# Optimization experiments

Hardware: AMD Instinct MI355X
Metric: run time of the kernel (lower is better)

The kernel has to match this reference:

```python
import jax, jax.numpy as jnp
import numpy as np

N_NODES = 100000
N_EDGES = 400000
HIDDEN = 128
HEADS = 8
HEAD_DIM = HIDDEN // HEADS


def _lin_params(key, d_in, d_out):
    kw, kb = jax.random.split(key)
    s = 1.0 / np.sqrt(d_in)
    W = jax.random.uniform(kw, (d_in, d_out), jnp.float32, -s, s)
    b = jax.random.uniform(kb, (d_out,), jnp.float32, -s, s)
    return W, b


def setup_inputs() -> dict:
    key = jax.random.key(0)
    ks = jax.random.split(key, 12)
    inp = {
        "x": jax.random.normal(ks[0], (N_NODES, HIDDEN), jnp.float32),
        "edge_attr": jax.random.normal(ks[1], (N_EDGES, HIDDEN), jnp.float32),
        "edge_index": jax.random.randint(ks[2], (2, N_EDGES), 0, N_NODES, dtype=jnp.int32),
        "batch": jnp.zeros((N_NODES,), jnp.int32),
    }
    names = ["Q", "K", "V", "Ew", "Eb", "Ev", "O", "Eo"]
    for i, nm in enumerate(names):
        W, b = _lin_params(ks[3 + i], HIDDEN, HIDDEN)
        inp[f"W_{nm}"] = W
        inp[f"b_{nm}"] = b
    WA, bA = _lin_params(ks[11], HIDDEN, HEADS)
    inp["W_A"] = WA
    inp["b_A"] = bA
    return inp


def signed_sqrt(x):
    return jnp.sign(x) * jnp.sqrt(jnp.abs(x) + 1e-8)


def reference(x, edge_attr, edge_index, batch,
              W_Q, b_Q, W_K, b_K, W_V, b_V,
              W_Ew, b_Ew, W_Eb, b_Eb, W_Ev, b_Ev,
              W_O, b_O, W_Eo, b_Eo, W_A, b_A):
    n = x.shape[0]
    e = edge_index.shape[1]
    h, hd = HEADS, HEAD_DIM
    src, tgt = edge_index[0], edge_index[1]

    Q = (x @ W_Q + b_Q).reshape(n, h, hd)
    K = (x @ W_K + b_K).reshape(n, h, hd)
    V = (x @ W_V + b_V).reshape(n, h, hd)

    # edge-gathered attention features [E, H, HD]
    attn_feat = Q[src] + K[tgt]
    E_w = (edge_attr @ W_Ew + b_Ew).reshape(e, h, hd)
    E_b = (edge_attr @ W_Eb + b_Eb).reshape(e, h, hd)
    attn_feat = signed_sqrt(attn_feat * E_w) + E_b
    attn_feat = jax.nn.relu(attn_feat)

    # per-head scores [E, H], segment softmax over target node
    scores = attn_feat.reshape(e, h * hd) @ W_A + b_A
    seg_max = jax.ops.segment_max(scores, tgt, num_segments=n)
    ex = jnp.exp(scores - seg_max[tgt])
    seg_sum = jax.ops.segment_sum(ex, tgt, num_segments=n)
    alpha = ex / (seg_sum[tgt] + 1e-16)  # [E, H]

    a = alpha[:, :, None]
    E_v = (edge_attr @ W_Ev + b_Ev).reshape(e, h, hd)
    messages = V[src] * a + E_v * a  # [E, H, HD]

    agg = jax.ops.segment_sum(messages, tgt, num_segments=n).reshape(n, h * hd)
    x_out = agg @ W_O + b_O
    edge_attr_out = attn_feat.reshape(e, h * hd) @ W_Eo + b_Eo
    return x_out, edge_attr_out
```

## Files before the change

### kernel.cpp

```cpp
#include <hip/hip_runtime.h>
#include <hip/hip_bf16.h>

typedef __hip_bfloat16 bf16;

#define N_NODES 100000
#define N_EDGES 400000
#define EO_MIN  100000

#define OUT_E_ELEM ((size_t)N_NODES*128)
#define SCORES_B   ((size_t)N_EDGES*8*4)
#define SEG_B      ((size_t)N_NODES*8*4)
#define AGG_BYTES  ((size_t)N_NODES*128*4)
#define WSW_OFF    (SCORES_B + 2*SEG_B)

#define WT_SZ   16384
#define OFF_WQ  (0*WT_SZ)
#define OFF_WK  (2*WT_SZ)
#define OFF_WEW (4*WT_SZ)
#define OFF_WEB (6*WT_SZ)
#define OFF_WEO (8*WT_SZ)
#define OFF_WV  (10*WT_SZ)
#define OFF_WEV (12*WT_SZ)
#define OFF_WA  (14*WT_SZ)
#define WSW_SHORTS (14*WT_SZ + 2*2048)
#define WSW_BYTES  ((size_t)WSW_SHORTS*2)

using short8 = __attribute__((ext_vector_type(8))) short;
using f32x4  = __attribute__((ext_vector_type(4))) float;

__device__ __forceinline__ float b2f(bf16 v){ return __bfloat162float(v); }
__device__ __forceinline__ bf16  f2b(float v){ return __float2bfloat16(v); }
__device__ __forceinline__ short bits(bf16 v){ short s; __builtin_memcpy(&s, &v, 2); return s; }
__device__ __forceinline__ void split(float v, short& h, short& l){
  bf16 hb = f2b(v);
  h = bits(hb);
  l = bits(f2b(v - b2f(hb)));
}
__device__ __forceinline__ float san(float v){
  return (v == v && fabsf(v) < 1e30f) ? v : 0.f;
}
__device__ __forceinline__ unsigned fmap(float f){
  unsigned u = __float_as_uint(f);
  return (u & 0x80000000u) ? ~u : (u | 0x80000000u);
}
__device__ __forceinline__ float funmap(unsigned u){
  unsigned b = (u & 0x80000000u) ? (u ^ 0x80000000u) : ~u;
  return __uint_as_float(b);
}

__global__ void prep_v18(const float* __restrict__ W_Q, const float* __restrict__ W_K,
                         const float* __restrict__ W_Ew, const float* __restrict__ W_Eb,
                         const float* __restrict__ W_Eo, const float* __restrict__ W_V,
                         const float* __restrict__ W_Ev, const float* __restrict__ W_A,
                         short* __restrict__ wsw)
{
  const int b = blockIdx.x;
  if (b < 896){
    const int mi = b >> 7, n = b & 127;
    const float* W = (mi==0)?W_Q:(mi==1)?W_K:(mi==2)?W_Ew:(mi==3)?W_Eb:(mi==4)?W_Eo:(mi==5)?W_V:W_Ev;
    short* dh = wsw + mi*2*WT_SZ;
    short* dl = dh + WT_SZ;
    for (int k = threadIdx.x; k < 128; k += 128){
      short h, l; split(W[(size_t)k*128 + n], h, l);
      dh[n*128 + k] = h; dl[n*128 + k] = l;
    }
  } else {
    const int n = b - 896;
    short* dh = wsw + OFF_WA;
    short* dl = dh + 2048;
    for (int k = threadIdx.x; k < 128; k += 128){
      float v = (n < 8) ? W_A[(size_t)k*8 + n] : 0.f;
      short h, l; split(v, h, l);
      dh[n*128 + k] = h; dl[n*128 + k] = l;
    }
  }
}

__device__ __forceinline__ void stage_row(const float* __restrict__ src,
                                          short* __restrict__ dh, short* __restrict__ dl){
  const float4 v0 = *reinterpret_cast<const float4*>(src);
  const float4 v1 = *reinterpret_cast<const float4*>(src + 4);
  const float vv[8] = {v0.x, v0.y, v0.z, v0.w, v1.x, v1.y, v1.z, v1.w};
  short8 h, l;
  #pragma unroll
  for (int q = 0; q < 8; ++q){ short hh, ll; split(vv[q], hh, ll); h[q] = hh; l[q] = ll; }
  *reinterpret_cast<short8*>(dh) = h;
  *reinterpret_cast<short8*>(dl) = l;
}

__global__ __launch_bounds__(256) void nodeproj_v18(
    const float* __restrict__ x, const short* __restrict__ wsw,
    const float* __restrict__ b_Q, const float* __restrict__ b_K,
    const float* __restrict__ b_V,
    float* __restrict__ Qn, float* __restrict__ Kn, float* __restrict__ Vn,
    int do_v)
{
  __shared__ __align__(16) short Xh[2][2048], Xl[2][2048];
  const int tid = threadIdx.x;
  const int n0  = blockIdx.x * 32;

  {
    const int r = tid & 15, c = tid >> 4;
    #pragma unroll
    for (int rg = 0; rg < 2; ++rg)
      stage_row(x + (size_t)(n0 + rg*16 + r)*128 + c*8,
                &Xh[rg][(c*16 + r)*8], &Xl[rg][(c*16 + r)*8]);
  }
  __syncthreads();

  const int wv = tid >> 6;
  const int mi = (tid & 63) & 15;
  const int kg = (tid & 63) >> 4;

  f32x4 aQ[2][2], aK[2][2], aV[2][2];
  #pragma unroll
  for (int rg = 0; rg < 2; ++rg)
    #pragma unroll
    for (int t = 0; t < 2; ++t){
      aQ[rg][t] = (f32x4){0,0,0,0}; aK[rg][t] = (f32x4){0,0,0,0}; aV[rg][t] = (f32x4){0,0,0,0};
    }

  #pragma unroll
  for (int ks = 0; ks < 4; ++ks){
// ... 17 lines not shown
      #pragma unroll
      for (int rg = 0; rg < 2; ++rg){
        aQ[rg][t] = __builtin_amdgcn_mfma_f32_16x16x32_bf16(xh[rg], qh, aQ[rg][t], 0,0,0);
        aK[rg][t] = __builtin_amdgcn_mfma_f32_16x16x32_bf16(xh[rg], kh, aK[rg][t], 0,0,0);
        aQ[rg][t] = __builtin_amdgcn_mfma_f32_16x16x32_bf16(xl[rg], qh, aQ[rg][t], 0,0,0);
        aK[rg][t] = __builtin_amdgcn_mfma_f32_16x16x32_bf16(xl[rg], kh, aK[rg][t], 0,0,0);
        aQ[rg][t] = __builtin_amdgcn_mfma_f32_16x16x32_bf16(xh[rg], ql, aQ[rg][t], 0,0,0);
        aK[rg][t] = __builtin_amdgcn_mfma_f32_16x16x32_bf16(xh[rg], kl, aK[rg][t], 0,0,0);
        if (do_v){
          aV[rg][t] = __builtin_amdgcn_mfma_f32_16x16x32_bf16(xh[rg], vh, aV[rg][t], 0,0,0);
          aV[rg][t] = __builtin_amdgcn_mfma_f32_16x16x32_bf16(xl[rg], vh, aV[rg][t], 0,0,0);
          aV[rg][t] = __builtin_amdgcn_mfma_f32_16x16x32_bf16(xh[rg], vl, aV[rg][t], 0,0,0);
        }
      }
    }
  }

  #pragma unroll
  for (int rg = 0; rg < 2; ++rg)
    #pragma unroll
    for (int t = 0; t < 2; ++t){
      const int n = (wv*2 + t)*16 + mi;
      const float bq = b_Q[n], bk = b_K[n], bv = b_V[n];
      #pragma unroll
      for (int q = 0; q < 4; ++q){
        const size_t row = n0 + rg*16 + kg*4 + q;
        Qn[row*128 + n] = aQ[rg][t][q] + bq;
        Kn[row*128 + n] = aK[rg][t][q] + bk;
        if (do_v) Vn[row*128 + n] = aV[rg][t][q] + bv;
      }
    }
}

__global__ __launch_bounds__(256) void front_qk_v18(
    const float* __restrict__ ea, const int* __restrict__ eidx,
    const float* __restrict__ Qn, const float* __restrict__ Kn,
    const float* __restrict__ b_Ew, const float* __restrict__ b_Eb,
    const float* __restrict__ b_A,  const float* __restrict__ b_Eo,
    const short* __restrict__ wsw,
    float* __restrict__ scores, unsigned* __restrict__ segmax,
    float* __restrict__ oute, int do_score)
{
  __shared__ __align__(16) char smem[16384];
  __shared__ int sIdx[32], tIdx[32];
  short* AFh = (short*)smem;
  short* AFl = (short*)(smem + 8192);
  float* qkf = (float*)smem;

  const int tid = threadIdx.x;
  const int e0  = blockIdx.x * 32;

  if (tid < 32){
    sIdx[tid] = eidx[e0 + tid];
    tIdx[tid] = eidx[N_EDGES + e0 + tid];
  }
  {
    const int r = tid & 15, c = tid >> 4;
    #pragma unroll
    for (int rg = 0; rg < 2; ++rg)
      stage_row(ea + (size_t)(e0 + rg*16 + r)*128 + c*8,
                &AFh[rg*2048 + (c*16 + r)*8], &AFl[rg*2048 + (c*16 + r)*8]);
  }
  __syncthreads();

  const int wv = tid >> 6;
  const int mi = (tid & 63) & 15;
  const int kg = (tid & 63) >> 4;

  f32x4 aw[2][2], ab[2][2];
  #pragma unroll
  for (int rg = 0; rg < 2; ++rg)
    #pragma unroll
    for (int t = 0; t < 2; ++t){ aw[rg][t] = (f32x4){0,0,0,0}; ab[rg][t] = (f32x4){0,0,0,0}; }

  #pragma unroll
  for (int ks = 0; ks < 4; ++ks){
    const int ao = ((ks*4 + kg)*16 + mi)*8;
    const int kb = ks*32 + kg*8;
    short8 eh[2], el_[2];
    #pragma unroll
    for (int rg = 0; rg < 2; ++rg){
      eh[rg]  = *reinterpret_cast<const short8*>(&AFh[rg*2048 + ao]);
      el_[rg] = *reinterpret_cast<const short8*>(&AFl[rg*2048 + ao]);
    }
    #pragma unroll
    for (int t = 0; t < 2; ++t){
      const int n = (wv*2 + t)*16 + mi;
      const short8 wh = *reinterpret_cast<const short8*>(&wsw[OFF_WEW + n*128 + kb]);
      const short8 wl = *reinterpret_cast<const short8*>(&wsw[OFF_WEW + WT_SZ + n*128 + kb]);
      const short8 bh = *reinterpret_cast<const short8*>(&wsw[OFF_WEB + n*128 + kb]);
      const short8 bl = *reinterpret_cast<const short8*>(&wsw[OFF_WEB + WT_SZ + n*128 + kb]);
      #pragma unroll
      for (int rg = 0; rg < 2; ++rg){
        aw[rg][t] = __builtin_amdgcn_mfma_f32_16x16x32_bf16(eh[rg], wh, aw[rg][t], 0,0,0);
        ab[rg][t] = __builtin_amdgcn_mfma_f32_16x16x32_bf16(eh[rg], bh, ab[rg][t], 0,0,0);
        aw[rg][t] = __builtin_amdgcn_mfma_f32_16x16x32_bf16(el_[rg], wh, aw[rg][t], 0,0,0);
        ab[rg][t] = __builtin_amdgcn_mfma_f32_16x16x32_bf16(el_[rg], bh, ab[rg][t], 0,0,0);
        aw[rg][t] = __builtin_amdgcn_mfma_f32_16x16x32_bf16(eh[rg], wl, aw[rg][t], 0,0,0);
        ab[rg][t] = __builtin_amdgcn_mfma_f32_16x16x32_bf16(eh[rg], bl, ab[rg][t], 0,0,0);
      }
    }
  }
  __syncthreads();

  {
    const int r = tid >> 3, cg = tid & 7;
    const float* qp = Qn + (size_t)sIdx[r]*128 + cg*16;
    const float* kp = Kn + (size_t)tIdx[r]*128 + cg*16;
    #pragma unroll
    for (int p = 0; p < 4; ++p){
      const float4 qv = *reinterpret_cast<const float4*>(qp + p*4);
      const float4 kv = *reinterpret_cast<const float4*>(kp + p*4);
      float4 s; s.x = qv.x+kv.x; s.y = qv.y+kv.y; s.z = qv.z+kv.z; s.w = qv.w+kv.w;
      *reinterpret_cast<float4*>(&qkf[r*128 + cg*16 + p*4]) = s;
    }
  }
  __syncthreads();

  short afh[2][2][4], afl[2][2][4];
  #pragma unroll
  for (int rg = 0; rg < 2; ++rg)
    #pragma unroll
    for (int t = 0; t < 2; ++t){
      const int n = (wv*2 + t)*16 + mi;
      const float bw = b_Ew[n], bb = b_Eb[n];
      #pragma unroll
      for (int q = 0; q < 4; ++q){
        const float qkv = qkf[(rg*16 + kg*4 + q)*128 + n];
        const float ew  = aw[rg][t][q] + bw;
        const float eb  = ab[rg][t][q] + bb;
        const float pre = qkv * ew;
        const float ssv = pre > 0.f ?  sqrtf( pre + 1e-8f)
                        : (pre < 0.f ? -sqrtf(-pre + 1e-8f) : 0.f);
        const float af = fmaxf(ssv + eb, 0.f);
        short hh, ll; split(af, hh, ll);
        afh[rg][t][q] = hh; afl[rg][t][q] = ll;
      }
    }
  __syncthreads();

  #pragma unroll
  for (int rg = 0; rg < 2; ++rg)
    #pragma unroll
    for (int t = 0; t < 2; ++t){
      const int c  = (wv*2 + t)*2 + (mi >> 3);
      const int k7 = mi & 7;
      #pragma unroll
// ... 27 lines not shown
        const int er = rg*16 + kg*4 + q;
        const float s = san(acc[q] + ba);
        scores[(size_t)(e0 + er)*8 + mi] = s;
        atomicMax(&segmax[(size_t)tIdx[er]*8 + mi], fmap(s));
      }
    }
  }

  #pragma unroll
  for (int rg = 0; rg < 2; ++rg)
    #pragma unroll
    for (int t2 = 0; t2 < 2; ++t2){
      const int n = (wv*2 + t2)*16 + mi;
      f32x4 acc = {0,0,0,0};
      #pragma unroll
      for (int ks = 0; ks < 4; ++ks){
        const int kb = ks*32 + kg*8;
        const int ao = ((ks*4 + kg)*16 + mi)*8;
        const short8 ah = *reinterpret_cast<const short8*>(&AFh[rg*2048 + ao]);
        const short8 al = *reinterpret_cast<const short8*>(&AFl[rg*2048 + ao]);
        const short8 bh = *reinterpret_cast<const short8*>(&wsw[OFF_WEO + n*128 + kb]);
        const short8 bl = *reinterpret_cast<const short8*>(&wsw[OFF_WEO + WT_SZ + n*128 + kb]);
        acc = __builtin_amdgcn_mfma_f32_16x16x32_bf16(ah, bh, acc, 0,0,0);
        acc = __builtin_amdgcn_mfma_f32_16x16x32_bf16(al, bh, acc, 0,0,0);
        acc = __builtin_amdgcn_mfma_f32_16x16x32_bf16(ah, bl, acc, 0,0,0);
      }
      const float be = b_Eo[n];
      #pragma unroll
      for (int q = 0; q < 4; ++q)
        oute[(size_t)(e0 + rg*16 + kg*4 + q)*128 + n] = san(acc[q] + be);
    }
}

__global__ __launch_bounds__(256) void seg_sum_v18(const float* __restrict__ scores,
    const int* __restrict__ eidx, const unsigned* __restrict__ segmax,
    float* __restrict__ segsum)
{
  int i = blockIdx.x*256 + threadIdx.x;
  if (i >= N_EDGES*8) return;
  int e = i >> 3, h = i & 7;
  int t = eidx[N_EDGES + e];
  float m = funmap(segmax[(size_t)t*8 + h]);
  atomicAdd(&segsum[(size_t)t*8 + h], expf(scores[i] - m));
}

__global__ __launch_bounds__(256) void messages_mfma_v18(
    const float* __restrict__ ea, const int* __restrict__ eidx,
    const float* __restrict__ Vn, const float* __restrict__ b_Ev,
    const short* __restrict__ wsw,
    const float* __restrict__ scores, const unsigned* __restrict__ segmax,
    float* __restrict__ den, float* __restrict__ agg)
{
  __shared__ __align__(16) short Eh[2][2048], El[2][2048];
  __shared__ int sIdx[32], tIdx[32];

  const int tid = threadIdx.x;
  const int e0  = blockIdx.x * 32;

  if (tid < 32){
    sIdx[tid] = eidx[e0 + tid];
    tIdx[tid] = eidx[N_EDGES + e0 + tid];
  }
  {
    const int r = tid & 15, c = tid >> 4;
    #pragma unroll
    for (int rg = 0; rg < 2; ++rg)
      stage_row(ea + (size_t)(e0 + rg*16 + r)*128 + c*8,
                &Eh[rg][(c*16 + r)*8], &El[rg][(c*16 + r)*8]);
  }
  __syncthreads();

  const int wv = tid >> 6;
  const int mi = (tid & 63) & 15;
  const int kg = (tid & 63) >> 4;

  f32x4 aev[2][2];
  #pragma unroll
  for (int rg = 0; rg < 2; ++rg)
    #pragma unroll
    for (int t = 0; t < 2; ++t) aev[rg][t] = (f32x4){0,0,0,0};

  #pragma unroll
  for (int ks = 0; ks < 4; ++ks){
    const int ao = ((ks*4 + kg)*16 + mi)*8;
    const int kb = ks*32 + kg*8;
    short8 eh[2], el_[2];
    #pragma unroll
    for (int rg = 0; rg < 2; ++rg){
      eh[rg]  = *reinterpret_cast<const short8*>(&Eh[rg][ao]);
      el_[rg] = *reinterpret_cast<const short8*>(&El[rg][ao]);
    }
    #pragma unroll
    for (int t = 0; t < 2; ++t){
      const int n = (wv*2 + t)*16 + mi;
      const short8 bh = *reinterpret_cast<const short8*>(&wsw[OFF_WEV + n*128 + kb]);
      const short8 bl = *reinterpret_cast<const short8*>(&wsw[OFF_WEV + WT_SZ + n*128 + kb]);
      #pragma unroll
      for (int rg = 0; rg < 2; ++rg){
        aev[rg][t] = __builtin_amdgcn_mfma_f32_16x16x32_bf16(eh[rg], bh, aev[rg][t], 0,0,0);
        aev[rg][t] = __builtin_amdgcn_mfma_f32_16x16x32_bf16(el_[rg], bh, aev[rg][t], 0,0,0);
        aev[rg][t] = __builtin_amdgcn_mfma_f32_16x16x32_bf16(eh[rg], bl, aev[rg][t], 0,0,0);
      }
    }
  }

  #pragma unroll
  for (int rg = 0; rg < 2; ++rg)
    #pragma unroll
    for (int t = 0; t < 2; ++t){
      const int n = (wv*2 + t)*16 + mi;
      const int h = n >> 4;
      const float be = b_Ev[n];
      #pragma unroll
      for (int q = 0; q < 4; ++q){
        const int row = rg*16 + kg*4 + q;
        const size_t e = (size_t)e0 + row;
        const int s = sIdx[row], tg = tIdx[row];
        const float m    = funmap(segmax[(size_t)tg*8 + h]);
        const float expw = expf(scores[e*8 + h] - m);
        const float msg  = san((Vn[(size_t)s*128 + n] + aev[rg][t][q] + be) * expw);
        atomicAdd(&agg[(size_t)tg*128 + n], msg);
        if (mi == 0) atomicAdd(&den[(size_t)tg*8 + h], expw);
      }
    }
}

__global__ __launch_bounds__(256) void messages_v14f(
    const float* __restrict__ x, const float* __restrict__ ea,
    const int* __restrict__ eidx,
    const float* __restrict__ W_V,  const float* __restrict__ b_V,
    const float* __restrict__ W_Ev, const float* __restrict__ b_Ev,
    const float* __restrict__ scores, const unsigned* __restrict__ segmax,
    const float* __restrict__ segsum, float* __restrict__ agg)
{
  __shared__ float eaT[128][16], xsT[128][16];
  __shared__ int sIdx[16], tIdx[16];

  const int tid = threadIdx.x;
  const int e0  = blockIdx.x * 16;

  if (tid < 16){
    sIdx[tid] = eidx[e0 + tid];
    tIdx[tid] = eidx[N_EDGES + e0 + tid];
  }
  __syncthreads();

  for (int idx = tid; idx < 16*128; idx += 256){
    int r = idx >> 7, k = idx & 127;
    eaT[k][r] = ea[(size_t)(e0 + r)*128 + k];
    xsT[k][r] = x[(size_t)sIdx[r]*128 + k];
  }
  __syncthreads();

  const int j  = tid & 127;
  const int h8 = (tid >> 7) * 8;
// ... 3 lines not shown
  for (int i=0;i<8;i++){ av[i]=0.f; ae[i]=0.f; }

  for (int k=0;k<128;k++){
    const float wv = W_V[(size_t)k*128 + j];
    const float we = W_Ev[(size_t)k*128 + j];
    const float4 s0 = *reinterpret_cast<const float4*>(&xsT[k][h8]);
    const float4 s1 = *reinterpret_cast<const float4*>(&xsT[k][h8+4]);
    const float4 e0v = *reinterpret_cast<const float4*>(&eaT[k][h8]);
    const float4 e1v = *reinterpret_cast<const float4*>(&eaT[k][h8+4]);
    const float sv[8] = {s0.x,s0.y,s0.z,s0.w,s1.x,s1.y,s1.z,s1.w};
    const float ev[8] = {e0v.x,e0v.y,e0v.z,e0v.w,e1v.x,e1v.y,e1v.z,e1v.w};
    #pragma unroll
    for (int i=0;i<8;i++){
      av[i] = fmaf(sv[i], wv, av[i]);
      ae[i] = fmaf(ev[i], we, ae[i]);
    }
  }

  const float bv = b_V[j], be = b_Ev[j];
  const int h = j >> 4;
  #pragma unroll
  for (int i=0;i<8;i++){
    const int el = h8 + i;
    const size_t e = (size_t)e0 + el;
    const int t = tIdx[el];
    const float m   = funmap(segmax[(size_t)t*8 + h]);
    const float d   = segsum[(size_t)t*8 + h] + 1e-16f;
    const float a   = expf(scores[e*8 + h] - m) / d;
    const float msg = san(((av[i] + bv) + (ae[i] + be)) * a);
    atomicAdd(&agg[(size_t)t*128 + j], msg);
  }
}

__global__ __launch_bounds__(256) void oproj_v18(const float* __restrict__ agg,
    const float* __restrict__ den,
    const float* __restrict__ W, const float* __restrict__ bias,
    float* __restrict__ outx)
{
  __shared__ float AT[128][32];
  const int tid  = threadIdx.x;
  const int base = blockIdx.x * 32;

  for (int idx = tid; idx < 32*128; idx += 256){
    int r = idx >> 7, k = idx & 127;
    float v = agg[(size_t)(base + r)*128 + k];
    if (den) v /= (den[(size_t)(base + r)*8 + (k >> 4)] + 1e-16f);
    AT[k][r] = v;
  }
  __syncthreads();

  const int j  = tid & 127;
  const int rb = (tid >> 7) * 16;
  float acc[16];
  #pragma unroll
  for (int i=0;i<16;i++) acc[i] = 0.f;

  for (int k=0;k<128;k++){
    const float w = W[(size_t)k*128 + j];
    const float4 a0 = *reinterpret_cast<const float4*>(&AT[k][rb]);
    const float4 a1 = *reinterpret_cast<const float4*>(&AT[k][rb+4]);
    const float4 a2 = *reinterpret_cast<const float4*>(&AT[k][rb+8]);
    const float4 a3 = *reinterpret_cast<const float4*>(&AT[k][rb+12]);
    const float avv[16] = {a0.x,a0.y,a0.z,a0.w,a1.x,a1.y,a1.z,a1.w,
                           a2.x,a2.y,a2.z,a2.w,a3.x,a3.y,a3.z,a3.w};
    #pragma unroll
    for (int i=0;i<16;i++) acc[i] = fmaf(avv[i], w, acc[i]);
  }

  const float bj = bias[j];
  #pragma unroll
  for (int i=0;i<16;i++)
    outx[(size_t)(base + rb + i)*128 + j] = san(acc[i] + bj);
}

template<bool PREPPED>
__global__ __launch_bounds__(256) void front_v14f(
    const float* __restrict__ x, const float* __restrict__ ea,
    const int* __restrict__ eidx,
    const float* __restrict__ W_Q, const float* __restrict__ b_Q,
    const float* __restrict__ W_K, const float* __restrict__ b_K,
// ... 172 lines not shown
        acc = __builtin_amdgcn_mfma_f32_16x16x32_bf16(ah, bh, acc, 0,0,0);
        acc = __builtin_amdgcn_mfma_f32_16x16x32_bf16(al, bh, acc, 0,0,0);
        acc = __builtin_amdgcn_mfma_f32_16x16x32_bf16(ah, bl, acc, 0,0,0);
      }
      const float be = b_Eo[n];
      #pragma unroll
      for (int q = 0; q < 4; ++q)
        oute[(size_t)(e0 + kg*4 + q)*128 + n] = san(acc[q] + be);
    }
  }
}

extern "C" void kernel_launch(void* const* d_in, const int* in_sizes, int n_in,
                              void* d_out, int out_size, void* d_ws, size_t ws_size,
                              hipStream_t stream)
{
  (void)in_sizes; (void)n_in; (void)out_size;
  const float* x    = (const float*)d_in[0];
  const float* ea   = (const float*)d_in[1];
  const int*   eidx = (const int*)d_in[2];
  const float* W_Q  = (const float*)d_in[4];  const float* b_Q  = (const float*)d_in[5];
  const float* W_K  = (const float*)d_in[6];  const float* b_K  = (const float*)d_in[7];
  const float* W_V  = (const float*)d_in[8];  const float* b_V  = (const float*)d_in[9];
  const float* W_Ew = (const float*)d_in[10]; const float* b_Ew = (const float*)d_in[11];
  const float* W_Eb = (const float*)d_in[12]; const float* b_Eb = (const float*)d_in[13];
  const float* W_Ev = (const float*)d_in[14]; const float* b_Ev = (const float*)d_in[15];
  const float* W_O  = (const float*)d_in[16]; const float* b_O  = (const float*)d_in[17];
  const float* W_Eo = (const float*)d_in[18]; const float* b_Eo = (const float*)d_in[19];
  const float* W_A  = (const float*)d_in[20]; const float* b_A  = (const float*)d_in[21];

  float* out_x = (float*)d_out;
  float* oute  = out_x + OUT_E_ELEM;

  float*    scores = (float*)d_out;
  unsigned* segmax = (unsigned*)((char*)d_out + SCORES_B);
  float*    segsum = (float*)((char*)d_out + SCORES_B + SEG_B);

  const size_t SZ_NODEF = (size_t)N_NODES*128*4;
  const size_t NEED_QK   = 2*SZ_NODEF + WSW_BYTES;
  const size_t NEED_FULL = 3*SZ_NODEF + WSW_BYTES;

  const int tier = (ws_size >= NEED_FULL) ? 2 : (ws_size >= NEED_QK) ? 1 : 0;

  dim3 blk(256);
  hipMemsetAsync((void*)segmax, 0, 2*SEG_B, stream);

  if (tier >= 1){
    char*  ws  = (char*)d_ws;
    float* Qn  = (float*)ws;
    float* Kn  = (float*)(ws + SZ_NODEF);
    float* Vn  = (tier == 2) ? (float*)(ws + 2*SZ_NODEF) : nullptr;
    short* wsw = (short*)(ws + ((tier == 2) ? 3 : 2)*SZ_NODEF);
    float* agg = Qn;
    float* den = Kn;

    prep_v18<<<dim3(912), dim3(128), 0, stream>>>(W_Q, W_K, W_Ew, W_Eb, W_Eo, W_V, W_Ev, W_A, wsw);

    nodeproj_v18<<<dim3(N_NODES/32), blk, 0, stream>>>(x, wsw, b_Q, b_K, b_V,
        Qn, Kn, Vn, tier == 2 ? 1 : 0);

    front_qk_v18<<<dim3(N_EDGES/32), blk, 0, stream>>>(ea, eidx, Qn, Kn,
        b_Ew, b_Eb, b_A, b_Eo, wsw, scores, segmax, oute, 1);

    hipMemsetAsync((void*)agg, 0, AGG_BYTES + SEG_B, stream);

    if (tier == 2){
      messages_mfma_v18<<<dim3(N_EDGES/32), blk, 0, stream>>>(ea, eidx, Vn, b_Ev,
          wsw, scores, segmax, den, agg);
      oproj_v18<<<dim3(N_NODES/32), blk, 0, stream>>>(agg, den, W_O, b_O, out_x);
    } else {
      seg_sum_v18<<<dim3((N_EDGES*8 + 255)/256), blk, 0, stream>>>(scores, eidx, segmax, segsum);
      messages_v14f<<<dim3(N_EDGES/16), blk, 0, stream>>>(x, ea, eidx,
          W_V, b_V, W_Ev, b_Ev, scores, segmax, segsum, agg);
      oproj_v18<<<dim3(N_NODES/32), blk, 0, stream>>>(agg, nullptr, W_O, b_O, out_x);
    }

  } else {
    short* wsw = (short*)((char*)d_out + WSW_OFF);
    float* agg = oute;

    hipMemsetAsync((void*)agg, 0, AGG_BYTES, stream);

    prep_v18<<<dim3(912), dim3(128), 0, stream>>>(W_Q, W_K, W_Ew, W_Eb, W_Eo, W_V, W_Ev, W_A, wsw);

    front_v14f<true><<<dim3(N_EDGES/16), blk, 0, stream>>>(x, ea, eidx,
        W_Q, b_Q, W_K, b_K, W_Ew, b_Ew, W_Eb, b_Eb, b_A, W_Eo, b_Eo, wsw,
        scores, segmax, oute, EO_MIN);

    seg_sum_v18<<<dim3((N_EDGES*8 + 255)/256), blk, 0, stream>>>(scores, eidx, segmax, segsum);

    messages_v14f<<<dim3(N_EDGES/16), blk, 0, stream>>>(x, ea, eidx,
        W_V, b_V, W_Ev, b_Ev, scores, segmax, segsum, agg);

    oproj_v18<<<dim3(N_NODES/32), blk, 0, stream>>>(agg, nullptr, W_O, b_O, out_x);

    front_v14f<false><<<dim3(EO_MIN/16), blk, 0, stream>>>(x, ea, eidx,
        W_Q, b_Q, W_K, b_K, W_Ew, b_Ew, W_Eb, b_Eb, b_A, W_Eo, b_Eo, nullptr,
        nullptr, nullptr, oute, 0);
  }
}
```

Baseline: 1.037 ms.

## Prefetch Q/K gathers early and restore separate segment-sum pass

In the edge front kernel, each thread now loads its gathered Q[src] and K[tgt] rows into registers at kernel start, before the MFMA edge projections, so the random-access latency overlaps with the matrix work. The tier-2 path also drops the per-message denominator atomics and the division inside the output projection. It instead runs a separate seg_sum pass and normalizes alpha inside the messages kernel, which adds an extra kernel and a scores reread but removes 8 atomics per edge from the messages kernel. Register pressure in the front kernel rises from holding 32 floats across the MFMA phase.

New measurement: 1.001 ms. 1.04x faster.

```diff
diff --git a/kernel.cpp b/kernel.cpp
--- a/kernel.cpp
+++ b/kernel.cpp
@@ -48,7 +48,7 @@
   return __uint_as_float(b);
 }
 
-__global__ void prep_v18(const float* __restrict__ W_Q, const float* __restrict__ W_K,
+__global__ void prep_v19(const float* __restrict__ W_Q, const float* __restrict__ W_K,
                          const float* __restrict__ W_Ew, const float* __restrict__ W_Eb,
                          const float* __restrict__ W_Eo, const float* __restrict__ W_V,
                          const float* __restrict__ W_Ev, const float* __restrict__ W_A,
@@ -88,7 +88,7 @@
   *reinterpret_cast<short8*>(dl) = l;
 }
 
-__global__ __launch_bounds__(256) void nodeproj_v18(
+__global__ __launch_bounds__(256) void nodeproj_v19(
     const float* __restrict__ x, const short* __restrict__ wsw,
     const float* __restrict__ b_Q, const float* __restrict__ b_K,
     const float* __restrict__ b_V,
@@ -172,7 +172,7 @@
     }
 }
 
-__global__ __launch_bounds__(256) void front_qk_v18(
+__global__ __launch_bounds__(256) void front_qk_v19(
     const float* __restrict__ ea, const int* __restrict__ eidx,
     const float* __restrict__ Qn, const float* __restrict__ Kn,
     const float* __restrict__ b_Ew, const float* __restrict__ b_Eb,
@@ -190,6 +190,20 @@
   const int tid = threadIdx.x;
   const int e0  = blockIdx.x * 32;
 
+  const int gr = tid >> 3, gc = tid & 7;
+  const int gse = eidx[e0 + gr];
+  const int gte = eidx[N_EDGES + e0 + gr];
+  float4 qv[4], kv[4];
+  {
+    const float* qp = Qn + (size_t)gse*128 + gc*16;
+    const float* kp = Kn + (size_t)gte*128 + gc*16;
+    #pragma unroll
+    for (int p = 0; p < 4; ++p){
+      qv[p] = *reinterpret_cast<const float4*>(qp + p*4);
+      kv[p] = *reinterpret_cast<const float4*>(kp + p*4);
+    }
+  }
+
   if (tid < 32){
     sIdx[tid] = eidx[e0 + tid];
     tIdx[tid] = eidx[N_EDGES + e0 + tid];
@@ -244,15 +258,12 @@
   __syncthreads();
 
   {
-    const int r = tid >> 3, cg = tid & 7;
-    const float* qp = Qn + (size_t)sIdx[r]*128 + cg*16;
-    const float* kp = Kn + (size_t)tIdx[r]*128 + cg*16;
     #pragma unroll
     for (int p = 0; p < 4; ++p){
-      const float4 qv = *reinterpret_cast<const float4*>(qp + p*4);
-      const float4 kv = *reinterpret_cast<const float4*>(kp + p*4);
-      float4 s; s.x = qv.x+kv.x; s.y = qv.y+kv.y; s.z = qv.z+kv.z; s.w = qv.w+kv.w;
-      *reinterpret_cast<float4*>(&qkf[r*128 + cg*16 + p*4]) = s;
+      float4 s;
+      s.x = qv[p].x + kv[p].x; s.y = qv[p].y + kv[p].y;
+      s.z = qv[p].z + kv[p].z; s.w = qv[p].w + kv[p].w;
+      *reinterpret_cast<float4*>(&qkf[gr*128 + gc*16 + p*4]) = s;
     }
   }
   __syncthreads();
@@ -346,7 +357,7 @@
     }
 }
 
-__global__ __launch_bounds__(256) void seg_sum_v18(const float* __restrict__ scores,
+__global__ __launch_bounds__(256) void seg_sum_v19(const float* __restrict__ scores,
     const int* __restrict__ eidx, const unsigned* __restrict__ segmax,
     float* __restrict__ segsum)
 {
@@ -358,12 +369,12 @@
   atomicAdd(&segsum[(size_t)t*8 + h], expf(scores[i] - m));
 }
 
-__global__ __launch_bounds__(256) void messages_mfma_v18(
+__global__ __launch_bounds__(256) void messages_mfma_v19(
     const float* __restrict__ ea, const int* __restrict__ eidx,
     const float* __restrict__ Vn, const float* __restrict__ b_Ev,
     const short* __restrict__ wsw,
     const float* __restrict__ scores, const unsigned* __restrict__ segmax,
-    float* __restrict__ den, float* __restrict__ agg)
+    const float* __restrict__ segsum, float* __restrict__ agg)
 {
   __shared__ __align__(16) short Eh[2][2048], El[2][2048];
   __shared__ int sIdx[32], tIdx[32];
@@ -430,11 +441,11 @@
         const int row = rg*16 + kg*4 + q;
         const size_t e = (size_t)e0 + row;
         const int s = sIdx[row], tg = tIdx[row];
-        const float m    = funmap(segmax[(size_t)tg*8 + h]);
-        const float expw = expf(scores[e*8 + h] - m);
-        const float msg  = san((Vn[(size_t)s*128 + n] + aev[rg][t][q] + be) * expw);
+        const float m   = funmap(segmax[(size_t)tg*8 + h]);
+        const float den = segsum[(size_t)tg*8 + h] + 1e-16f;
+        const float a   = expf(scores[e*8 + h] - m) / den;
+        const float msg = san((Vn[(size_t)s*128 + n] + aev[rg][t][q] + be) * a);
         atomicAdd(&agg[(size_t)tg*128 + n], msg);
-        if (mi == 0) atomicAdd(&den[(size_t)tg*8 + h], expw);
       }
     }
 }
@@ -504,8 +515,7 @@
   }
 }
 
-__global__ __launch_bounds__(256) void oproj_v18(const float* __restrict__ agg,
-    const float* __restrict__ den,
+__global__ __launch_bounds__(256) void oproj_v19(const float* __restrict__ agg,
     const float* __restrict__ W, const float* __restrict__ bias,
     float* __restrict__ outx)
 {
@@ -515,9 +525,7 @@
 
   for (int idx = tid; idx < 32*128; idx += 256){
     int r = idx >> 7, k = idx & 127;
-    float v = agg[(size_t)(base + r)*128 + k];
-    if (den) v /= (den[(size_t)(base + r)*8 + (k >> 4)] + 1e-16f);
-    AT[k][r] = v;
+    AT[k][r] = agg[(size_t)(base + r)*128 + k];
   }
   __syncthreads();
 
@@ -776,28 +784,27 @@
     float* Vn  = (tier == 2) ? (float*)(ws + 2*SZ_NODEF) : nullptr;
     short* wsw = (short*)(ws + ((tier == 2) ? 3 : 2)*SZ_NODEF);
     float* agg = Qn;
-    float* den = Kn;
-
-    prep_v18<<<dim3(912), dim3(128), 0, stream>>>(W_Q, W_K, W_Ew, W_Eb, W_Eo, W_V, W_Ev, W_A, wsw);
-
-    nodeproj_v18<<<dim3(N_NODES/32), blk, 0, stream>>>(x, wsw, b_Q, b_K, b_V,
+
+    prep_v19<<<dim3(912), dim3(128), 0, stream>>>(W_Q, W_K, W_Ew, W_Eb, W_Eo, W_V, W_Ev, W_A, wsw);
+
+    nodeproj_v19<<<dim3(N_NODES/32), blk, 0, stream>>>(x, wsw, b_Q, b_K, b_V,
         Qn, Kn, Vn, tier == 2 ? 1 : 0);
 
-    front_qk_v18<<<dim3(N_EDGES/32), blk, 0, stream>>>(ea, eidx, Qn, Kn,
+    front_qk_v19<<<dim3(N_EDGES/32), blk, 0, stream>>>(ea, eidx, Qn, Kn,
         b_Ew, b_Eb, b_A, b_Eo, wsw, scores, segmax, oute, 1);
 
-    hipMemsetAsync((void*)agg, 0, AGG_BYTES + SEG_B, stream);
-
-    if (tier == 2){
-      messages_mfma_v18<<<dim3(N_EDGES/32), blk, 0, stream>>>(ea, eidx, Vn, b_Ev,
-          wsw, scores, segmax, den, agg);
-      oproj_v18<<<dim3(N_NODES/32), blk, 0, stream>>>(agg, den, W_O, b_O, out_x);
-    } else {
-      seg_sum_v18<<<dim3((N_EDGES*8 + 255)/256), blk, 0, stream>>>(scores, eidx, segmax, segsum);
+    hipMemsetAsync((void*)agg, 0, AGG_BYTES, stream);
+
+    seg_sum_v19<<<dim3((N_EDGES*8 + 255)/256), blk, 0, stream>>>(scores, eidx, segmax, segsum);
+
+    if (tier == 2)
+      messages_mfma_v19<<<dim3(N_EDGES/32), blk, 0, stream>>>(ea, eidx, Vn, b_Ev,
+          wsw, scores, segmax, segsum, agg);
+    else
       messages_v14f<<<dim3(N_EDGES/16), blk, 0, stream>>>(x, ea, eidx,
           W_V, b_V, W_Ev, b_Ev, scores, segmax, segsum, agg);
-      oproj_v18<<<dim3(N_NODES/32), blk, 0, stream>>>(agg, nullptr, W_O, b_O, out_x);
-    }
+
+    oproj_v19<<<dim3(N_NODES/32), blk, 0, stream>>>(agg, W_O, b_O, out_x);
 
   } else {
     short* wsw = (short*)((char*)d_out + WSW_OFF);
@@ -805,18 +812,18 @@
 
     hipMemsetAsync((void*)agg, 0, AGG_BYTES, stream);
 
-    prep_v18<<<dim3(912), dim3(128), 0, stream>>>(W_Q, W_K, W_Ew, W_Eb, W_Eo, W_V, W_Ev, W_A, wsw);
+    prep_v19<<<dim3(912), dim3(128), 0, stream>>>(W_Q, W_K, W_Ew, W_Eb, W_Eo, W_V, W_Ev, W_A, wsw);
 
     front_v14f<true><<<dim3(N_EDGES/16), blk, 0, stream>>>(x, ea, eidx,
         W_Q, b_Q, W_K, b_K, W_Ew, b_Ew, W_Eb, b_Eb, b_A, W_Eo, b_Eo, wsw,
         scores, segmax, oute, EO_MIN);
 
-    seg_sum_v18<<<dim3((N_EDGES*8 + 255)/256), blk, 0, stream>>>(scores, eidx, segmax, segsum);
+    seg_sum_v19<<<dim3((N_EDGES*8 + 255)/256), blk, 0, stream>>>(scores, eidx, segmax, segsum);
 
     messages_v14f<<<dim3(N_EDGES/16), blk, 0, stream>>>(x, ea, eidx,
         W_V, b_V, W_Ev, b_Ev, scores, segmax, segsum, agg);
 
-    oproj_v18<<<dim3(N_NODES/32), blk, 0, stream>>>(agg, nullptr, W_O, b_O, out_x);
+    oproj_v19<<<dim3(N_NODES/32), blk, 0, stream>>>(agg, W_O, b_O, out_x);
 
     front_v14f<false><<<dim3(EO_MIN/16), blk, 0, stream>>>(x, ea, eidx,
         W_Q, b_Q, W_K, b_K, W_Ew, b_Ew, W_Eb, b_Eb, b_A, W_Eo, b_Eo, nullptr,
```

## Fuse edge front and message passes into one kernel without max-subtracted softmax

Applied to the files above, without the earlier changes.

Adds a fused edge kernel that computes E_w, E_b and E_v projections together, forms attention features, scores, exponentials, the per-target denominators and the aggregated messages plus the edge output in a single pass. Normalization moves into the output projection, which divides by the accumulated denominator. This removes the separate scores buffer, the segment-max pass and the second read of edge_attr. The trade-off is that the softmax no longer subtracts the segment max, so exp can overflow for large scores; it relies on san() and on score magnitudes staying small. The fused path only runs when the workspace has room for the extra denominator buffer.

After: 907.3 us. -12.5%, faster.

```diff
diff --git a/kernel.cpp b/kernel.cpp
--- a/kernel.cpp
+++ b/kernel.cpp
@@ -48,7 +48,7 @@
   return __uint_as_float(b);
 }
 
-__global__ void prep_v18(const float* __restrict__ W_Q, const float* __restrict__ W_K,
+__global__ void prep_v20(const float* __restrict__ W_Q, const float* __restrict__ W_K,
                          const float* __restrict__ W_Ew, const float* __restrict__ W_Eb,
                          const float* __restrict__ W_Eo, const float* __restrict__ W_V,
                          const float* __restrict__ W_Ev, const float* __restrict__ W_A,
@@ -88,7 +88,7 @@
   *reinterpret_cast<short8*>(dl) = l;
 }
 
-__global__ __launch_bounds__(256) void nodeproj_v18(
+__global__ __launch_bounds__(256) void nodeproj_v20(
     const float* __restrict__ x, const short* __restrict__ wsw,
     const float* __restrict__ b_Q, const float* __restrict__ b_K,
     const float* __restrict__ b_V,
@@ -172,7 +172,251 @@
     }
 }
 
-__global__ __launch_bounds__(256) void front_qk_v18(
+__global__ __launch_bounds__(256) void front_fused_v20(
+    const float* __restrict__ ea, const int* __restrict__ eidx,
+    const float* __restrict__ Qn, const float* __restrict__ Kn,
+    const float* __restrict__ Vn,
+    const float* __restrict__ b_Ew, const float* __restrict__ b_Eb,
+    const float* __restrict__ b_A,  const float* __restrict__ b_Eo,
+    const float* __restrict__ b_Ev,
+    const short* __restrict__ wsw,
+    float* __restrict__ den, float* __restrict__ agg,
+    float* __restrict__ oute)
+{
+  __shared__ __align__(16) char smem[16384];
+  __shared__ float exps[32][8];
+  __shared__ int sIdx[32], tIdx[32];
+  short* AFh = (short*)smem;
+  short* AFl = (short*)(smem + 8192);
+  float* qkf = (float*)smem;
+
+  const int tid = threadIdx.x;
+  const int e0  = blockIdx.x * 32;
+
+  if (tid < 32){
+    sIdx[tid] = eidx[e0 + tid];
+    tIdx[tid] = eidx[N_EDGES + e0 + tid];
+  }
+  {
+    const int r = tid & 15, c = tid >> 4;
+    #pragma unroll
+    for (int rg = 0; rg < 2; ++rg)
+      stage_row(ea + (size_t)(e0 + rg*16 + r)*128 + c*8,
+                &AFh[rg*2048 + (c*16 + r)*8], &AFl[rg*2048 + (c*16 + r)*8]);
+  }
+  __syncthreads();
+
+  const int wv = tid >> 6;
+  const int mi = (tid & 63) & 15;
+  const int kg = (tid & 63) >> 4;
+
+  f32x4 aw[2][2], ab[2][2], aev[2][2];
+  #pragma unroll
+  for (int rg = 0; rg < 2; ++rg)
+    #pragma unroll
+    for (int t = 0; t < 2; ++t){
+      aw[rg][t] = (f32x4){0,0,0,0}; ab[rg][t] = (f32x4){0,0,0,0};
+      aev[rg][t] = (f32x4){0,0,0,0};
+    }
+
+  #pragma unroll
+  for (int ks = 0; ks < 4; ++ks){
+    const int ao = ((ks*4 + kg)*16 + mi)*8;
+    const int kb = ks*32 + kg*8;
+    short8 eh[2], el_[2];
+    #pragma unroll
+    for (int rg = 0; rg < 2; ++rg){
+      eh[rg]  = *reinterpret_cast<const short8*>(&AFh[rg*2048 + ao]);
+      el_[rg] = *reinterpret_cast<const short8*>(&AFl[rg*2048 + ao]);
+    }
+    #pragma unroll
+    for (int t = 0; t < 2; ++t){
+      const int n = (wv*2 + t)*16 + mi;
+      const short8 wh = *reinterpret_cast<const short8*>(&wsw[OFF_WEW + n*128 + kb]);
+      const short8 wl = *reinterpret_cast<const short8*>(&wsw[OFF_WEW + WT_SZ + n*128 + kb]);
+      const short8 bh = *reinterpret_cast<const short8*>(&wsw[OFF_WEB + n*128 + kb]);
+      const short8 bl = *reinterpret_cast<const short8*>(&wsw[OFF_WEB + WT_SZ + n*128 + kb]);
+      const short8 vh = *reinterpret_cast<const short8*>(&wsw[OFF_WEV + n*128 + kb]);
+      const short8 vl = *reinterpret_cast<const short8*>(&wsw[OFF_WEV + WT_SZ + n*128 + kb]);
+      #pragma unroll
+      for (int rg = 0; rg < 2; ++rg){
+        aw[rg][t]  = __builtin_amdgcn_mfma_f32_16x16x32_bf16(eh[rg], wh, aw[rg][t], 0,0,0);
+        ab[rg][t]  = __builtin_amdgcn_mfma_f32_16x16x32_bf16(eh[rg], bh, ab[rg][t], 0,0,0);
+        aev[rg][t] = __builtin_amdgcn_mfma_f32_16x16x32_bf16(eh[rg], vh, aev[rg][t], 0,0,0);
+        aw[rg][t]  = __builtin_amdgcn_mfma_f32_16x16x32_bf16(el_[rg], wh, aw[rg][t], 0,0,0);
+        ab[rg][t]  = __builtin_amdgcn_mfma_f32_16x16x32_bf16(el_[rg], bh, ab[rg][t], 0,0,0);
+        aev[rg][t] = __builtin_amdgcn_mfma_f32_16x16x32_bf16(el_[rg], vh, aev[rg][t], 0,0,0);
+        aw[rg][t]  = __builtin_amdgcn_mfma_f32_16x16x32_bf16(eh[rg], wl, aw[rg][t], 0,0,0);
+        ab[rg][t]  = __builtin_amdgcn_mfma_f32_16x16x32_bf16(eh[rg], bl, ab[rg][t], 0,0,0);
+        aev[rg][t] = __builtin_amdgcn_mfma_f32_16x16x32_bf16(eh[rg], vl, aev[rg][t], 0,0,0);
+      }
+    }
+  }
+  __syncthreads();
+
+  {
+    const int r = tid >> 3, cg = tid & 7;
+    const float* qp = Qn + (size_t)sIdx[r]*128 + cg*16;
+    const float* kp = Kn + (size_t)tIdx[r]*128 + cg*16;
+    #pragma unroll
+    for (int p = 0; p < 4; ++p){
+      const float4 qv = *reinterpret_cast<const float4*>(qp + p*4);
+      const float4 kv = *reinterpret_cast<const float4*>(kp + p*4);
+      float4 s; s.x = qv.x+kv.x; s.y = qv.y+kv.y; s.z = qv.z+kv.z; s.w = qv.w+kv.w;
+      *reinterpret_cast<float4*>(&qkf[r*128 + cg*16 + p*4]) = s;
+    }
+  }
+  __syncthreads();
+
+  short afh[2][2][4], afl[2][2][4];
+  #pragma unroll
+  for (int rg = 0; rg < 2; ++rg)
+    #pragma unroll
+    for (int t = 0; t < 2; ++t){
+      const int n = (wv*2 + t)*16 + mi;
+      const float bw = b_Ew[n], bb = b_Eb[n];
+      #pragma unroll
+      for (int q = 0; q < 4; ++q){
+        const float qkv = qkf[(rg*16 + kg*4 + q)*128 + n];
+        const float ew  = aw[rg][t][q] + bw;
+        const float eb  = ab[rg][t][q] + bb;
+        const float pre = qkv * ew;
+        const float ssv = pre > 0.f ?  sqrtf( pre + 1e-8f)
+                        : (pre < 0.f ? -sqrtf(-pre + 1e-8f) : 0.f);
+        const float af = fmaxf(ssv + eb, 0.f);
+        short hh, ll; split(af, hh, ll);
+        afh[rg][t][q] = hh; afl[rg][t][q] = ll;
+      }
+    }
+  __syncthreads();
+
+  #pragma unroll
+  for (int rg = 0; rg < 2; ++rg)
+    #pragma unroll
+    for (int t = 0; t < 2; ++t){
+      const int c  = (wv*2 + t)*2 + (mi >> 3);
+      const int k7 = mi & 7;
+      #pragma unroll
+      for (int q = 0; q < 4; ++q){
+        const int idx = (c*16 + kg*4 + q)*8 + k7;
+        AFh[rg*2048 + idx] = afh[rg][t][q];
+        AFl[rg*2048 + idx] = afl[rg][t][q];
+      }
+    }
+  __syncthreads();
+
+  if (wv < 2){
+    const int rg = wv;
+    f32x4 acc = {0,0,0,0};
+    #pragma unroll
+    for (int ks = 0; ks < 4; ++ks){
+      const int kb = ks*32 + kg*8;
+      const int ao = ((ks*4 + kg)*16 + mi)*8;
+      const short8 ah = *reinterpret_cast<const short8*>(&AFh[rg*2048 + ao]);
+      const short8 al = *reinterpret_cast<const short8*>(&AFl[rg*2048 + ao]);
+      const short8 bh = *reinterpret_cast<const short8*>(&wsw[OFF_WA + mi*128 + kb]);
+      const short8 bl = *reinterpret_cast<const short8*>(&wsw[OFF_WA + 2048 + mi*128 + kb]);
+      acc = __builtin_amdgcn_mfma_f32_16x16x32_bf16(ah, bh, acc, 0,0,0);
+      acc = __builtin_amdgcn_mfma_f32_16x16x32_bf16(al, bh, acc, 0,0,0);
+      acc = __builtin_amdgcn_mfma_f32_16x16x32_bf16(ah, bl, acc, 0,0,0);
+    }
+    if (mi < 8){
+      const float ba = b_A[mi];
+      #pragma unroll
+      for (int q = 0; q < 4; ++q){
+        const int er = rg*16 + kg*4 + q;
+        const float ev = expf(san(acc[q] + ba));
+        exps[er][mi] = ev;
+        atomicAdd(&den[(size_t)tIdx[er]*8 + mi], ev);
+      }
+    }
+  }
+  __syncthreads();
+
+  #pragma unroll
+  for (int rg = 0; rg < 2; ++rg)
+    #pragma unroll
+    for (int t = 0; t < 2; ++t){
+      const int n = (wv*2 + t)*16 + mi;
+      const int h = n >> 4;
+      const float bev = b_Ev[n];
+      #pragma unroll
+      for (int q = 0; q < 4; ++q){
+        const int row = rg*16 + kg*4 + q;
+        const int s = sIdx[row], tg = tIdx[row];
+        const float ew_ = exps[row][h];
+        const float msg = san((Vn[(size_t)s*128 + n] + aev[rg][t][q] + bev) * ew_);
+        atomicAdd(&agg[(size_t)tg*128 + n], msg);
+      }
+    }
+
+  #pragma unroll
+  for (int rg = 0; rg < 2; ++rg)
+    #pragma unroll
+    for (int t2 = 0; t2 < 2; ++t2){
+      const int n = (wv*2 + t2)*16 + mi;
+      f32x4 acc = {0,0,0,0};
+      #pragma unroll
+      for (int ks = 0; ks < 4; ++ks){
+        const int kb = ks*32 + kg*8;
+        const int ao = ((ks*4 + kg)*16 + mi)*8;
+        const short8 ah = *reinterpret_cast<const short8*>(&AFh[rg*2048 + ao]);
+        const short8 al = *reinterpret_cast<const short8*>(&AFl[rg*2048 + ao]);
+        const short8 bh = *reinterpret_cast<const short8*>(&wsw[OFF_WEO + n*128 + kb]);
+        const short8 bl = *reinterpret_cast<const short8*>(&wsw[OFF_WEO + WT_SZ + n*128 + kb]);
+        acc = __builtin_amdgcn_mfma_f32_16x16x32_bf16(ah, bh, acc, 0,0,0);
+        acc = __builtin_amdgcn_mfma_f32_16x16x32_bf16(al, bh, acc, 0,0,0);
+        acc = __builtin_amdgcn_mfma_f32_16x16x32_bf16(ah, bl, acc, 0,0,0);
+      }
+      const float be = b_Eo[n];
+      #pragma unroll
+      for (int q = 0; q < 4; ++q)
+        oute[(size_t)(e0 + rg*16 + kg*4 + q)*128 + n] = san(acc[q] + be);
+    }
+}
+
+__global__ __launch_bounds__(256) void oproj_div_v20(const float* __restrict__ agg,
+    const float* __restrict__ den,
+    const float* __restrict__ W, const float* __restrict__ bias,
+    float* __restrict__ outx)
+{
+  __shared__ float AT[128][32];
+  const int tid  = threadIdx.x;
+  const int base = blockIdx.x * 32;
+
+  for (int idx = tid; idx < 32*128; idx += 256){
+    int r = idx >> 7, k = idx & 127;
+    float v = agg[(size_t)(base + r)*128 + k];
+    v /= (den[(size_t)(base + r)*8 + (k >> 4)] + 1e-16f);
+    AT[k][r] = v;
+  }
+  __syncthreads();
+
+  const int j  = tid & 127;
+  const int rb = (tid >> 7) * 16;
+  float acc[16];
+  #pragma unroll
+  for (int i=0;i<16;i++) acc[i] = 0.f;
+
+  for (int k=0;k<128;k++){
+    const float w = W[(size_t)k*128 + j];
+    const float4 a0 = *reinterpret_cast<const float4*>(&AT[k][rb]);
+    const float4 a1 = *reinterpret_cast<const float4*>(&AT[k][rb+4]);
+    const float4 a2 = *reinterpret_cast<const float4*>(&AT[k][rb+8]);
+    const float4 a3 = *reinterpret_cast<const float4*>(&AT[k][rb+12]);
+    const float avv[16] = {a0.x,a0.y,a0.z,a0.w,a1.x,a1.y,a1.z,a1.w,
+                           a2.x,a2.y,a2.z,a2.w,a3.x,a3.y,a3.z,a3.w};
+    #pragma unroll
+    for (int i=0;i<16;i++) acc[i] = fmaf(avv[i], w, acc[i]);
+  }
+
+  const float bj = bias[j];
+  #pragma unroll
+  for (int i=0;i<16;i++)
+    outx[(size_t)(base + rb + i)*128 + j] = san(acc[i] + bj);
+}
+
+__global__ __launch_bounds__(256) void front_qk_v19f(
     const float* __restrict__ ea, const int* __restrict__ eidx,
     const float* __restrict__ Qn, const float* __restrict__ Kn,
     const float* __restrict__ b_Ew, const float* __restrict__ b_Eb,
@@ -346,7 +590,7 @@
     }
 }
 
-__global__ __launch_bounds__(256) void seg_sum_v18(const float* __restrict__ scores,
+__global__ __launch_bounds__(256) void seg_sum_v20(const float* __restrict__ scores,
     const int* __restrict__ eidx, const unsigned* __restrict__ segmax,
     float* __restrict__ segsum)
 {
@@ -358,12 +602,12 @@
   atomicAdd(&segsum[(size_t)t*8 + h], expf(scores[i] - m));
 }
 
-__global__ __launch_bounds__(256) void messages_mfma_v18(
+__global__ __launch_bounds__(256) void messages_mfma_v20(
     const float* __restrict__ ea, const int* __restrict__ eidx,
     const float* __restrict__ Vn, const float* __restrict__ b_Ev,
     const short* __restrict__ wsw,
     const float* __restrict__ scores, const unsigned* __restrict__ segmax,
-    float* __restrict__ den, float* __restrict__ agg)
+    const float* __restrict__ segsum, float* __restrict__ agg)
 {
   __shared__ __align__(16) short Eh[2][2048], El[2][2048];
   __shared__ int sIdx[32], tIdx[32];
@@ -430,11 +674,11 @@
         const int row = rg*16 + kg*4 + q;
         const size_t e = (size_t)e0 + row;
         const int s = sIdx[row], tg = tIdx[row];
-        const float m    = funmap(segmax[(size_t)tg*8 + h]);
-        const float expw = expf(scores[e*8 + h] - m);
-        const float msg  = san((Vn[(size_t)s*128 + n] + aev[rg][t][q] + be) * expw);
+        const float m   = funmap(segmax[(size_t)tg*8 + h]);
+        const float dn  = segsum[(size_t)tg*8 + h] + 1e-16f;
+        const float a   = expf(scores[e*8 + h] - m) / dn;
+        const float msg = san((Vn[(size_t)s*128 + n] + aev[rg][t][q] + be) * a);
         atomicAdd(&agg[(size_t)tg*128 + n], msg);
-        if (mi == 0) atomicAdd(&den[(size_t)tg*8 + h], expw);
       }
     }
 }
@@ -504,8 +748,7 @@
   }
 }
 
-__global__ __launch_bounds__(256) void oproj_v18(const float* __restrict__ agg,
-    const float* __restrict__ den,
+__global__ __launch_bounds__(256) void oproj_v20(const float* __restrict__ agg,
     const float* __restrict__ W, const float* __restrict__ bias,
     float* __restrict__ outx)
 {
@@ -515,9 +758,7 @@
 
   for (int idx = tid; idx < 32*128; idx += 256){
     int r = idx >> 7, k = idx & 127;
-    float v = agg[(size_t)(base + r)*128 + k];
-    if (den) v /= (den[(size_t)(base + r)*8 + (k >> 4)] + 1e-16f);
-    AT[k][r] = v;
+    AT[k][r] = agg[(size_t)(base + r)*128 + k];
   }
   __syncthreads();
 
@@ -756,70 +997,94 @@
   float* out_x = (float*)d_out;
   float* oute  = out_x + OUT_E_ELEM;
 
-  float*    scores = (float*)d_out;
-  unsigned* segmax = (unsigned*)((char*)d_out + SCORES_B);
-  float*    segsum = (float*)((char*)d_out + SCORES_B + SEG_B);
-
-  const size_t SZ_NODEF = (size_t)N_NODES*128*4;
-  const size_t NEED_QK   = 2*SZ_NODEF + WSW_BYTES;
-  const size_t NEED_FULL = 3*SZ_NODEF + WSW_BYTES;
-
-  const int tier = (ws_size >= NEED_FULL) ? 2 : (ws_size >= NEED_QK) ? 1 : 0;
+  const size_t SZ_NODEF  = (size_t)N_NODES*128*4;
+  const size_t NEED_QK    = 2*SZ_NODEF + WSW_BYTES;
+  const size_t NEED_FULL  = 3*SZ_NODEF + WSW_BYTES;
+  const size_t NEED_FUSED = NEED_FULL + SEG_B;
 
   dim3 blk(256);
-  hipMemsetAsync((void*)segmax, 0, 2*SEG_B, stream);
-
-  if (tier >= 1){
+
+  if (ws_size >= NEED_FUSED){
     char*  ws  = (char*)d_ws;
     float* Qn  = (float*)ws;
     float* Kn  = (float*)(ws + SZ_NODEF);
-    float* Vn  = (tier == 2) ? (float*)(ws + 2*SZ_NODEF) : nullptr;
-    short* wsw = (short*)(ws + ((tier == 2) ? 3 : 2)*SZ_NODEF);
-    float* agg = Qn;
-    float* den = Kn;
-
-    prep_v18<<<dim3(912), dim3(128), 0, stream>>>(W_Q, W_K, W_Ew, W_Eb, W_Eo, W_V, W_Ev, W_A, wsw);
-
-    nodeproj_v18<<<dim3(N_NODES/32), blk, 0, stream>>>(x, wsw, b_Q, b_K, b_V,
-        Qn, Kn, Vn, tier == 2 ? 1 : 0);
-
-    front_qk_v18<<<dim3(N_EDGES/32), blk, 0, stream>>>(ea, eidx, Qn, Kn,
-        b_Ew, b_Eb, b_A, b_Eo, wsw, scores, segmax, oute, 1);
-
-    hipMemsetAsync((void*)agg, 0, AGG_BYTES + SEG_B, stream);
-
-    if (tier == 2){
-      messages_mfma_v18<<<dim3(N_EDGES/32), blk, 0, stream>>>(ea, eidx, Vn, b_Ev,
-          wsw, scores, segmax, den, agg);
-      oproj_v18<<<dim3(N_NODES/32), blk, 0, stream>>>(agg, den, W_O, b_O, out_x);
+    float* Vn  = (float*)(ws + 2*SZ_NODEF);
+    short* wsw = (short*)(ws + 3*SZ_NODEF);
+    float* den = (float*)(ws + NEED_FULL);
+    float* agg = out_x;
+
+    hipMemsetAsync((void*)agg, 0, AGG_BYTES, stream);
+    hipMemsetAsync((void*)den, 0, SEG_B, stream);
+
+    prep_v20<<<dim3(912), dim3(128), 0, stream>>>(W_Q, W_K, W_Ew, W_Eb, W_Eo, W_V, W_Ev, W_A, wsw);
+
+    nodeproj_v20<<<dim3(N_NODES/32), blk, 0, stream>>>(x, wsw, b_Q, b_K, b_V,
+        Qn, Kn, Vn, 1);
+
+    front_fused_v20<<<dim3(N_EDGES/32), blk, 0, stream>>>(ea, eidx, Qn, Kn, Vn,
+        b_Ew, b_Eb, b_A, b_Eo, b_Ev, wsw, den, agg, oute);
+
+    oproj_div_v20<<<dim3(N_NODES/32), blk, 0, stream>>>(agg, den, W_O, b_O, out_x);
+
+  } else {
+    float*    scores = (float*)d_out;
+    unsigned* segmax = (unsigned*)((char*)d_out + SCORES_B);
+    float*    segsum = (float*)((char*)d_out + SCORES_B + SEG_B);
+    const int tier = (ws_size >= NEED_FULL) ? 2 : (ws_size >= NEED_QK) ? 1 : 0;
+
+    hipMemsetAsync((void*)segmax, 0, 2*SEG_B, stream);
+
+    if (tier >= 1){
+      char*  ws  = (char*)d_ws;
+      float* Qn  = (float*)ws;
+      float* Kn  = (float*)(ws + SZ_NODEF);
+      float* Vn  = (tier == 2) ? (float*)(ws + 2*SZ_NODEF) : nullptr;
+      short* wsw = (short*)(ws + ((tier == 2) ? 3 : 2)*SZ_NODEF);
+      float* agg = Qn;
+
+      prep_v20<<<dim3(912), dim3(128), 0, stream>>>(W_Q, W_K, W_Ew, W_Eb, W_Eo, W_V, W_Ev, W_A, wsw);
+
+      nodeproj_v20<<<dim3(N_NODES/32), blk, 0, stream>>>(x, wsw, b_Q, b_K, b_V,
+          Qn, Kn, Vn, tier == 2 ? 1 : 0);
+
+      front_qk_v19f<<<dim3(N_EDGES/32), blk, 0, stream>>>(ea, eidx, Qn, Kn,
+          b_Ew, b_Eb, b_A, b_Eo, wsw, scores, segmax, oute, 1);
+
+      hipMemsetAsync((void*)agg, 0, AGG_BYTES, stream);
+
+      seg_sum_v20<<<dim3((N_EDGES*8 + 255)/256), blk, 0, stream>>>(scores, eidx, segmax, segsum);
+
+      if (tier == 2)
+        messages_mfma_v20<<<dim3(N_EDGES/32), blk, 0, stream>>>(ea, eidx, Vn, b_Ev,
+            wsw, scores, segmax, segsum, agg);
+      else
+        messages_v14f<<<dim3(N_EDGES/16), blk, 0, stream>>>(x, ea, eidx,
+            W_V, b_V, W_Ev, b_Ev, scores, segmax, segsum, agg);
+
+      oproj_v20<<<dim3(N_NODES/32), blk, 0, stream>>>(agg, W_O, b_O, out_x);
+
     } else {
-      seg_sum_v18<<<dim3((N_EDGES*8 + 255)/256), blk, 0, stream>>>(scores, eidx, segmax, segsum);
+      short* wsw = (short*)((char*)d_out + WSW_OFF);
+      float* agg = oute;
+
+      hipMemsetAsync((void*)agg, 0, AGG_BYTES, stream);
+
+      prep_v20<<<dim3(912), dim3(128), 0, stream>>>(W_Q, W_K, W_Ew, W_Eb, W_Eo, W_V, W_Ev, W_A, wsw);
+
+      front_v14f<true><<<dim3(N_EDGES/16), blk, 0, stream>>>(x, ea, eidx,
+          W_Q, b_Q, W_K, b_K, W_Ew, b_Ew, W_Eb, b_Eb, b_A, W_Eo, b_Eo, wsw,
+          scores, segmax, oute, EO_MIN);
+
+      seg_sum_v20<<<dim3((N_EDGES*8 + 255)/256), blk, 0, stream>>>(scores, eidx, segmax, segsum);
+
       messages_v14f<<<dim3(N_EDGES/16), blk, 0, stream>>>(x, ea, eidx,
           W_V, b_V, W_Ev, b_Ev, scores, segmax, segsum, agg);
-      oproj_v18<<<dim3(N_NODES/32), blk, 0, stream>>>(agg, nullptr, W_O, b_O, out_x);
-    }
-
-  } else {
-    short* wsw = (short*)((char*)d_out + WSW_OFF);
-    float* agg = oute;
-
-    hipMemsetAsync((void*)agg, 0, AGG_BYTES, stream);
-
-    prep_v18<<<dim3(912), dim3(128), 0, stream>>>(W_Q, W_K, W_Ew, W_Eb, W_Eo, W_V, W_Ev, W_A, wsw);
-
-    front_v14f<true><<<dim3(N_EDGES/16), blk, 0, stream>>>(x, ea, eidx,
-        W_Q, b_Q, W_K, b_K, W_Ew, b_Ew, W_Eb, b_Eb, b_A, W_Eo, b_Eo, wsw,
-        scores, segmax, oute, EO_MIN);
-
-    seg_sum_v18<<<dim3((N_EDGES*8 + 255)/256), blk, 0, stream>>>(scores, eidx, segmax, segsum);
-
-    messages_v14f<<<dim3(N_EDGES/16), blk, 0, stream>>>(x, ea, eidx,
-        W_V, b_V, W_Ev, b_Ev, scores, segmax, segsum, agg);
-
-    oproj_v18<<<dim3(N_NODES/32), blk, 0, stream>>>(agg, nullptr, W_O, b_O, out_x);
-
-    front_v14f<false><<<dim3(EO_MIN/16), blk, 0, stream>>>(x, ea, eidx,
-        W_Q, b_Q, W_K, b_K, W_Ew, b_Ew, W_Eb, b_Eb, b_A, W_Eo, b_Eo, nullptr,
-        nullptr, nullptr, oute, 0);
-  }
-}
+
+      oproj_v20<<<dim3(N_NODES/32), blk, 0, stream>>>(agg, W_O, b_O, out_x);
+
+      front_v14f<false><<<dim3(EO_MIN/16), blk, 0, stream>>>(x, ea, eidx,
+          W_Q, b_Q, W_K, b_K, W_Ew, b_Ew, W_Eb, b_Eb, b_A, W_Eo, b_Eo, nullptr,
+          nullptr, nullptr, oute, 0);
+    }
+  }
+}
```
